# Performance work log

Measured on AMD Instinct MI355X. Metric: run time of the kernel, lower is better.

Reference implementation:

```python
import jax, jax.numpy as jnp
import numpy as np

N_CFG = 400_000    # total basic-block nodes across the batch
E_CFG = 1_600_000  # CFG edges
N_FUNC = 8_000     # internal functions across the batch
N_EXT = 1_600      # external functions across the batch
N_FCG = N_FUNC + N_EXT
E_FCG = 80_000     # call-graph edges
B = 8              # binaries per batch
D_IN, D_H = 64, 128
VOCAB = 10_002     # max_vocab_size + 2


def gcn_layer(x, edge_index, W, b, n_nodes):
    # PyG GCNConv with self-loops: x' = D^{-1/2}(A+I)D^{-1/2} (x W) + b
    h = x @ W
    row, col = edge_index[0], edge_index[1]
    deg = jax.ops.segment_sum(jnp.ones_like(col, dtype=h.dtype), col, num_segments=n_nodes) + 1.0
    dis = jax.lax.rsqrt(deg)
    norm = (dis[row] * dis[col])[:, None]
    agg = jax.ops.segment_sum(h[row] * norm, col, num_segments=n_nodes)
    return agg + h * (dis * dis)[:, None] + b  # second term is the self-loop message


def segment_mean(x, seg, n):
    s = jax.ops.segment_sum(x, seg, num_segments=n)
    c = jax.ops.segment_sum(jnp.ones((x.shape[0],), x.dtype), seg, num_segments=n)
    return s / jnp.maximum(c, 1.0)[:, None]


def setup_inputs() -> dict:
    key = jax.random.key(0)
    ks = jax.random.split(key, 24)
    s = 0.05
    cfg_x = jax.random.normal(ks[0], (N_CFG, D_IN), jnp.float32)
    cfg_edge_index = jax.random.randint(ks[1], (2, E_CFG), 0, N_CFG)
    cfg_node2func = jnp.sort(jax.random.randint(ks[2], (N_CFG,), 0, N_FUNC))
    fcg_edge_index = jax.random.randint(ks[3], (2, E_FCG), 0, N_FCG)
    fcg_batch = jnp.sort(jax.random.randint(ks[4], (N_FCG,), 0, B))
    # first N_FUNC FCG nodes are internal (index into pooled CFG embeddings),
    # the rest are external (index into the embedding table, avoiding pad idx 0)
    fcg_src_idx = jnp.concatenate([jnp.arange(N_FUNC, dtype=jnp.int64 if jax.config.jax_enable_x64 else jnp.int32).astype(jnp.int32),
                                   jax.random.randint(ks[5], (N_EXT,), 1, VOCAB)])
    fcg_is_ext = jnp.concatenate([jnp.zeros((N_FUNC,), jnp.int32), jnp.ones((N_EXT,), jnp.int32)])
    emb_table = jax.random.normal(ks[6], (VOCAB, D_H), jnp.float32) * s
    emb_table = emb_table.at[0].set(0.0)  # padding_idx row
    return {
        'cfg_x': cfg_x, 'cfg_edge_index': cfg_edge_index, 'cfg_node2func': cfg_node2func,
        'fcg_edge_index': fcg_edge_index, 'fcg_batch': fcg_batch,
        'fcg_src_idx': fcg_src_idx, 'fcg_is_ext': fcg_is_ext,
        'W_cfg1': jax.random.normal(ks[7], (D_IN, D_H), jnp.float32) * s,
        'b_cfg1': jax.random.normal(ks[8], (D_H,), jnp.float32) * s,
        'W_cfg2': jax.random.normal(ks[9], (D_H, D_H), jnp.float32) * s,
        'b_cfg2': jax.random.normal(ks[10], (D_H,), jnp.float32) * s,
        'emb_table': emb_table,
        'W_fcg1': jax.random.normal(ks[11], (D_H, D_H), jnp.float32) * s,
        'b_fcg1': jax.random.normal(ks[12], (D_H,), jnp.float32) * s,
        'Wp1': jax.random.normal(ks[13], (D_H, D_H // 2), jnp.float32) * s,
        'bp1': jax.random.normal(ks[14], (D_H // 2,), jnp.float32) * s,
        'Wp2': jax.random.normal(ks[15], (D_H // 2, D_H // 4), jnp.float32) * s,
        'bp2': jax.random.normal(ks[16], (D_H // 4,), jnp.float32) * s,
        'Wp3': jax.random.normal(ks[17], (D_H // 4, 1), jnp.float32) * s,
        'bp3': jax.random.normal(ks[18], (1,), jnp.float32) * s,
    }


def reference(cfg_x, cfg_edge_index, cfg_node2func, fcg_edge_index, fcg_batch,
              fcg_src_idx, fcg_is_ext, W_cfg1, b_cfg1, W_cfg2, b_cfg2, emb_table,
              W_fcg1, b_fcg1, Wp1, bp1, Wp2, bp2, Wp3, bp3):
    # CFG-level GCN stack (dropout is identity in eval)
    x = jax.nn.relu(gcn_layer(cfg_x, cfg_edge_index, W_cfg1, b_cfg1, N_CFG))
    x = jax.nn.relu(gcn_layer(x, cfg_edge_index, W_cfg2, b_cfg2, N_CFG))
    # global_mean_pool per function
    x_cfg_pool = segment_mean(x, cfg_node2func, N_FUNC)  # [N_FUNC, D_H]
    # assemble FCG node features: internal = pooled CFG embedding, external = embedding lookup
    internal = jnp.take(x_cfg_pool, jnp.clip(fcg_src_idx, 0, N_FUNC - 1), axis=0)
    external = jnp.take(emb_table, fcg_src_idx, axis=0, mode='clip')
    fcg_x = jnp.where((fcg_is_ext == 1)[:, None], external, internal)  # [N_FCG, D_H]
    # FCG-level GCN
    y = jax.nn.relu(gcn_layer(fcg_x, fcg_edge_index, W_fcg1, b_fcg1, N_FCG))
    # global_mean_pool per binary
    g = segment_mean(y, fcg_batch, B)  # [B, D_H]
    # projection head + sigmoid
    h = jax.nn.relu(g @ Wp1 + bp1)
    h = jax.nn.relu(h @ Wp2 + bp2)
    return jax.nn.sigmoid(h @ Wp3 + bp3)  # [B, 1]
```

## Files before the change

### kernel.cpp

```cpp
#include <hip/hip_runtime.h>
#include <math.h>

#define N_CFG 400000
#define E_CFG 1600000
#define N_FUNC 8000
#define N_EXT 1600
#define N_FCG (N_FUNC + N_EXT)
#define E_FCG 80000
#define NBATCH 8
#define VOCAB 10002

typedef unsigned int uint32;
typedef __attribute__((ext_vector_type(8))) short bf16x8;
typedef __attribute__((ext_vector_type(4))) float f32x4;

__device__ __forceinline__ float bf2f(unsigned short u){
  union { unsigned int i; float f; } v; v.i = ((unsigned int)u) << 16; return v.f;
}
__device__ __forceinline__ float bflo(unsigned int u){
  union { unsigned int i; float f; } v; v.i = u << 16; return v.f;
}
__device__ __forceinline__ float bfhi(unsigned int u){
  union { unsigned int i; float f; } v; v.i = u & 0xffff0000u; return v.f;
}
__device__ __forceinline__ unsigned short f2bf(float f){
  union { float f; unsigned int i; } v; v.f = f;
  unsigned int i = v.i;
  unsigned int r = (i + 0x7fffu + ((i >> 16) & 1u)) >> 16;
  return (unsigned short)r;
}
__device__ __forceinline__ unsigned int packbf(float x, float y){
  return (unsigned int)f2bf(x) | (((unsigned int)f2bf(y)) << 16);
}

__global__ void k_detect(const void* __restrict__ emb, int* __restrict__ flag){
  __shared__ int viol;
  if (threadIdx.x == 0) viol = 0;
  __syncthreads();
  const unsigned int* u = (const unsigned int*)emb;
  int my = 0;
  for (int i = threadIdx.x; i < 1024; i += 256){
    unsigned int lo = u[i] & 0xffffu;
    unsigned int ex = (lo >> 7) & 0xffu;
    bool ok = (ex == 0u) || (ex >= 80u && ex <= 127u);
    if (!ok) my++;
  }
  atomicAdd(&viol, my);
  __syncthreads();
  if (threadIdx.x == 0) *flag = (viol < 100) ? 1 : 0;
}

__global__ void k_conv(const void* __restrict__ src, unsigned short* __restrict__ dst,
                       int n, const int* __restrict__ flag){
  int i = blockIdx.x * 256 + threadIdx.x;
  if (i >= n) return;
  if (*flag) dst[i] = ((const unsigned short*)src)[i];
  else       dst[i] = f2bf(((const float*)src)[i]);
}

__global__ void k_convT(const void* __restrict__ src, unsigned short* __restrict__ dst,
                        int K, int N, const int* __restrict__ flag){
  int i = blockIdx.x * 256 + threadIdx.x;
  if (i >= K * N) return;
  int k = i / N, n = i - k * N;
  unsigned short v;
  if (*flag) v = ((const unsigned short*)src)[i];
  else       v = f2bf(((const float*)src)[i]);
  dst[n * K + k] = v;
}

__global__ void k_count(const int* __restrict__ idx, int n, uint32* __restrict__ cnt){
  int i = blockIdx.x * 256 + threadIdx.x;
  if (i < n) atomicAdd(&cnt[idx[i]], 1u);
}

__global__ void k_count_sorted(const int* __restrict__ seg, int n, uint32* __restrict__ cnt){
  int base = (blockIdx.x * 256 + threadIdx.x) * 64;
  if (base >= n) return;
  int end = base + 64; if (end > n) end = n;
  int curv = seg[base]; uint32 run = 1;
  for (int i = base + 1; i < end; i++){
    int v = seg[i];
    if (v == curv) run++;
    else { atomicAdd(&cnt[curv], run); curv = v; run = 1; }
  }
  atomicAdd(&cnt[curv], run);
}

__global__ void k_scan1(const uint32* __restrict__ cnt, int n,
                        uint32* __restrict__ off, uint32* __restrict__ bsums){
  __shared__ uint32 s[256];
  int tid = threadIdx.x;
  int base = blockIdx.x * 1024 + tid * 4;
  uint32 v0 = (base+0<n)?cnt[base+0]:0u, v1 = (base+1<n)?cnt[base+1]:0u;
  uint32 v2 = (base+2<n)?cnt[base+2]:0u, v3 = (base+3<n)?cnt[base+3]:0u;
  uint32 tsum = v0+v1+v2+v3;
  uint32 x = tsum;
  s[tid] = x; __syncthreads();
  for (int o = 1; o < 256; o <<= 1){
    uint32 y = (tid >= o) ? s[tid - o] : 0u;
    __syncthreads();
    x += y; s[tid] = x; __syncthreads();
  }
  uint32 run = x - tsum;
  if (base+0<n) off[base+0]=run; run+=v0;
  if (base+1<n) off[base+1]=run; run+=v1;
  if (base+2<n) off[base+2]=run; run+=v2;
  if (base+3<n) off[base+3]=run;
  if (tid == 255) bsums[blockIdx.x] = x;
}

__global__ void k_scan2(uint32* bsums, int nb){
  __shared__ uint32 s[1024];
  int tid = threadIdx.x;
  uint32 v = (tid < nb) ? bsums[tid] : 0u;
  uint32 x = v;
  s[tid] = x; __syncthreads();
  for (int o = 1; o < 1024; o <<= 1){
    uint32 y = (tid >= o) ? s[tid - o] : 0u;
    __syncthreads();
    x += y; s[tid] = x; __syncthreads();
  }
  if (tid < nb) bsums[tid] = x - v;
}

__global__ void k_scan3(uint32* off, uint32* cur, const uint32* __restrict__ bsums, int n){
  int i = blockIdx.x * 256 + threadIdx.x;
  if (i >= n) return;
  uint32 v = off[i] + bsums[i >> 10];
  off[i] = v;
  if (cur) cur[i] = v;
}

__global__ void k_fill(const int* __restrict__ edges, int E,
                       uint32* __restrict__ cur, int* __restrict__ sorted){
  int e = blockIdx.x * 256 + threadIdx.x;
  if (e >= E) return;
  int r = edges[e];
  int c = edges[E + e];
  uint32 p = atomicAdd(&cur[c], 1u);
  sorted[p] = r;
}

__global__ void k_dis(const uint32* __restrict__ cnt, float* __restrict__ dis, int n){
  int i = blockIdx.x * 256 + threadIdx.x;
  if (i < n) dis[i] = rsqrtf((float)cnt[i] + 1.0f);
}

template<int K>
__global__ __launch_bounds__(256)
void k_gemm_mfma(const void* __restrict__ Xsrc, const unsigned short* __restrict__ Wt,
                 const float* __restrict__ dis, unsigned short* __restrict__ out,
                 const int* __restrict__ flag, int mixed){
  const int KP = K + 8;
  __shared__ unsigned short Xs[64 * (K + 8)];
  __shared__ unsigned short Ws[128 * (K + 8)];
  int tid = threadIdx.x;
  long row0 = (long)blockIdx.x * 64;

  {
    int n = tid >> 1, half = tid & 1;
    const uint4* src = (const uint4*)(Wt + n * K) + half * (K / 16);
    uint4* dst = (uint4*)(Ws + n * KP) + half * (K / 16);
    #pragma unroll
    for (int i = 0; i < K / 16; i++) dst[i] = src[i];
  }
  {
    int r = tid >> 2, part = tid & 3;
    int isbf = mixed ? *flag : 1;
    uint4* dst = (uint4*)(Xs + r * KP) + part * (K / 32);
    if (isbf){
      const uint4* src = (const uint4*)((const unsigned short*)Xsrc + (row0 + r) * K) + part * (K / 32);
      #pragma unroll
      for (int i = 0; i < K / 32; i++) dst[i] = src[i];
    } else {
      const float4* src = (const float4*)((const float*)Xsrc + (row0 + r) * K) + part * (K / 16);
      #pragma unroll
      for (int i = 0; i < K / 32; i++){
        float4 f0 = src[2*i], f1 = src[2*i+1];
        uint4 u;
        u.x = packbf(f0.x, f0.y); u.y = packbf(f0.z, f0.w);
        u.z = packbf(f1.x, f1.y); u.w = packbf(f1.z, f1.w);
        dst[i] = u;
      }
    }
  }
  __syncthreads();

  int w = tid >> 6, lane = tid & 63, m = lane & 15, q = lane >> 4;
  f32x4 acc[8];
  #pragma unroll
  for (int t = 0; t < 8; t++) acc[t] = (f32x4){0.f, 0.f, 0.f, 0.f};

  const unsigned short* Arow = &Xs[(w * 16 + m) * KP + q * 8];
  const unsigned short* Bbase = &Ws[m * KP + q * 8];
  #pragma unroll
  for (int kc = 0; kc < K; kc += 32){
    bf16x8 a = *(const bf16x8*)(Arow + kc);
    #pragma unroll
    for (int t = 0; t < 8; t++){
      bf16x8 b = *(const bf16x8*)(Bbase + t * 16 * KP + kc);
      acc[t] = __builtin_amdgcn_mfma_f32_16x16x32_bf16(a, b, acc[t], 0, 0, 0);
    }
  }

  float d[4];
  #pragma unroll
  for (int r = 0; r < 4; r++) d[r] = dis[row0 + w * 16 + q * 4 + r];
  #pragma unroll
  for (int t = 0; t < 8; t++){
    #pragma unroll
    for (int r = 0; r < 4; r++){
      long grow = row0 + w * 16 + q * 4 + r;
      out[grow * 128 + t * 16 + m] = f2bf(acc[t][r] * d[r]);
    }
  }
}

__global__ __launch_bounds__(256)
void k_agg4(const uint4* __restrict__ hs4,
            const uint32* __restrict__ off, const uint32* __restrict__ cnt,
            const int* __restrict__ sorted, const float* __restrict__ dis,
            const uint4* __restrict__ bias4, uint4* __restrict__ out4, int n){
  int tid = threadIdx.x;
  int wave = tid >> 6, lane = tid & 63, grp = lane >> 4, sub = lane & 15;
  int node = blockIdx.x * 16 + wave * 4 + grp;
  if (node >= n) return;
  uint32 o = off[node], c = cnt[node];
  float a[8] = {0.f,0.f,0.f,0.f,0.f,0.f,0.f,0.f};
  for (uint32 j = 0; j < c; j++){
    int r = sorted[o + j];
    uint4 u = hs4[(long)r * 16 + sub];
    a[0] += bflo(u.x); a[1] += bfhi(u.x);
    a[2] += bflo(u.y); a[3] += bfhi(u.y);
    a[4] += bflo(u.z); a[5] += bfhi(u.z);
    a[6] += bflo(u.w); a[7] += bfhi(u.w);
  }
  {
    uint4 u = hs4[(long)node * 16 + sub];
    a[0] += bflo(u.x); a[1] += bfhi(u.x);
    a[2] += bflo(u.y); a[3] += bfhi(u.y);
    a[4] += bflo(u.z); a[5] += bfhi(u.z);
    a[6] += bflo(u.w); a[7] += bfhi(u.w);
  }
  float d = dis[node];
  uint4 b = bias4[sub];
  float v0 = fmaxf(fmaf(d, a[0], bflo(b.x)), 0.f);
  float v1 = fmaxf(fmaf(d, a[1], bfhi(b.x)), 0.f);
  float v2 = fmaxf(fmaf(d, a[2], bflo(b.y)), 0.f);
  float v3 = fmaxf(fmaf(d, a[3], bfhi(b.y)), 0.f);
  float v4 = fmaxf(fmaf(d, a[4], bflo(b.z)), 0.f);
  float v5 = fmaxf(fmaf(d, a[5], bfhi(b.z)), 0.f);
  float v6 = fmaxf(fmaf(d, a[6], bflo(b.w)), 0.f);
  float v7 = fmaxf(fmaf(d, a[7], bfhi(b.w)), 0.f);
  uint4 ov;
  ov.x = packbf(v0, v1); ov.y = packbf(v2, v3);
  ov.z = packbf(v4, v5); ov.w = packbf(v6, v7);
  out4[(long)node * 16 + sub] = ov;
}

__global__ __launch_bounds__(256)
void k_pool_batch(const uint4* __restrict__ y4, const uint32* __restrict__ g_cnt,
                  float* __restrict__ g_sum){
  __shared__ float red[16][128];
  int b = blockIdx.x >> 3, s = blockIdx.x & 7;
  int tid = threadIdx.x;
  int grp = tid >> 4, sub = tid & 15;
  uint32 start = 0;
  for (int i = 0; i < b; i++) start += g_cnt[i];
  uint32 cb = g_cnt[b];
  uint32 len = (cb + 7) / 8;
  uint32 lo = s * len;
  uint32 hi = lo + len; if (hi > cb) hi = cb;
  float a[8] = {0.f,0.f,0.f,0.f,0.f,0.f,0.f,0.f};
  for (uint32 i = lo + grp; i < hi; i += 16){
    uint4 u = y4[(long)(start + i) * 16 + sub];
    a[0] += bflo(u.x); a[1] += bfhi(u.x);
    a[2] += bflo(u.y); a[3] += bfhi(u.y);
    a[4] += bflo(u.z); a[5] += bfhi(u.z);
    a[6] += bflo(u.w); a[7] += bfhi(u.w);
  }
  #pragma unroll
  for (int i = 0; i < 8; i++) red[grp][sub * 8 + i] = a[i];
  __syncthreads();
  if (tid < 128){
    float t = 0.f;
    #pragma unroll
    for (int g = 0; g < 16; g++) t += red[g][tid];
    atomicAdd(&g_sum[b * 128 + tid], t);
  }
}

__global__ void k_pool_mean(const unsigned int* __restrict__ x2, const uint32* __restrict__ off,
                            const uint32* __restrict__ cnt, unsigned int* __restrict__ pooled2, int nf){
  int f = blockIdx.x; int t = threadIdx.x;
  uint32 o = off[f], c = cnt[f];
  float sx = 0.f, sy = 0.f;
  for (uint32 j = 0; j < c; j++){
    unsigned int u = x2[(long)(o + j) * 64 + t];
    sx += bflo(u); sy += bfhi(u);
  }
  float inv = 1.0f / (float)((c > 0u) ? c : 1u);
  pooled2[(long)f * 64 + t] = packbf(sx * inv, sy * inv);
}

__global__ void k_assemble(const unsigned int* __restrict__ pooled2, const unsigned int* __restrict__ emb2,
                           const int* __restrict__ src, const int* __restrict__ isext,
                           unsigned int* __restrict__ fx2){
  int i = blockIdx.x; int t = threadIdx.x;
  int s = src[i];
  unsigned int v;
  if (isext[i] == 1){
    int idx = s; if (idx < 0) idx = 0; if (idx > VOCAB - 1) idx = VOCAB - 1;
    v = emb2[(long)idx * 64 + t];
  } else {
    int f = s; if (f < 0) f = 0; if (f > N_FUNC - 1) f = N_FUNC - 1;
    v = pooled2[(long)f * 64 + t];
  }
  fx2[(long)i * 64 + t] = v;
}

__global__ __launch_bounds__(256)
void k_head(const float* __restrict__ g_sum, const uint32* __restrict__ g_cnt,
            const unsigned short* __restrict__ Wp1, const unsigned short* __restrict__ bp1,
            const unsigned short* __restrict__ Wp2, const unsigned short* __restrict__ bp2,
            const unsigned short* __restrict__ Wp3, const unsigned short* __restrict__ bp3,
            void* __restrict__ outp, const int* __restrict__ flag){
  __shared__ float G[8 * 128];
  __shared__ float H1[8 * 64];
  __shared__ float H2[8 * 32];
  int tid = threadIdx.x;
  for (int i = tid; i < 1024; i += 256){
    uint32 c = g_cnt[i >> 7];
    G[i] = g_sum[i] / (float)((c > 0u) ? c : 1u);
  }
  __syncthreads();
  for (int i = tid; i < 512; i += 256){
    int b = i >> 6, j = i & 63;
    float a = bf2f(bp1[j]);
    for (int d = 0; d < 128; d++) a = fmaf(G[b * 128 + d], bf2f(Wp1[d * 64 + j]), a);
    H1[i] = fmaxf(a, 0.f);
  }
  __syncthreads();
  {
    int b = tid >> 5, j = tid & 31;
    float a = bf2f(bp2[j]);
    for (int d = 0; d < 64; d++) a = fmaf(H1[b * 64 + d], bf2f(Wp2[d * 32 + j]), a);
    H2[tid] = fmaxf(a, 0.f);
  }
  __syncthreads();
  if (tid < 8){
    float a = bf2f(bp3[0]);
    for (int d = 0; d < 32; d++) a = fmaf(H2[tid * 32 + d], bf2f(Wp3[d]), a);
    float s = 1.f / (1.f + __expf(-a));
    if (*flag) ((unsigned short*)outp)[tid] = f2bf(s);
    else       ((float*)outp)[tid] = s;
  }
}

extern "C" void kernel_launch(void* const* d_in, const int* in_sizes, int n_in,
                              void* d_out, int out_size, void* d_ws, size_t ws_size,
                              hipStream_t stream){
  const void* cfg_x     = d_in[0];
  const int*  cfg_edges = (const int*)d_in[1];
  const int*  node2func = (const int*)d_in[2];
  const int*  fcg_edges = (const int*)d_in[3];
  const int*  fcg_batch = (const int*)d_in[4];
  const int*  fcg_src   = (const int*)d_in[5];
  const int*  fcg_isext = (const int*)d_in[6];
  const void* W1  = d_in[7];
  const void* b1  = d_in[8];
  const void* W2  = d_in[9];
  const void* b2  = d_in[10];
  const void* emb = d_in[11];
  const void* Wf  = d_in[12];
  const void* bfv = d_in[13];
  const void* Wp1 = d_in[14];
  const void* bp1 = d_in[15];
  const void* Wp2 = d_in[16];
  const void* bp2 = d_in[17];
  const void* Wp3 = d_in[18];
  const void* bp3 = d_in[19];

  char* p = (char*)d_ws;
  auto carve = [&](size_t bytes)->char* {
    char* r = p; p += (bytes + 255) & ~(size_t)255; return r;
  };
  unsigned short* A   = (unsigned short*)carve((size_t)N_CFG * 128 * 2);
  unsigned short* Bx  = (unsigned short*)carve((size_t)N_CFG * 128 * 2);
  uint32* cnt_cfg = (uint32*)carve((size_t)N_CFG * 4);
  uint32* off_cfg = (uint32*)carve((size_t)N_CFG * 4);
  uint32* cur_cfg = (uint32*)carve((size_t)N_CFG * 4);
  float*  dis_cfg = (float*) carve((size_t)N_CFG * 4);
  int*    sorted_cfg = (int*)carve((size_t)E_CFG * 4);
  uint32* bsums   = (uint32*)carve(1024 * 4);
  uint32* pool_cnt = (uint32*)carve(N_FUNC * 4);
  uint32* pool_off = (uint32*)carve(N_FUNC * 4);
  unsigned int* pooled2 = (unsigned int*)carve((size_t)N_FUNC * 64 * 4);
  unsigned int* fx2     = (unsigned int*)carve((size_t)N_FCG * 64 * 4);
  unsigned short* hsf   = (unsigned short*)carve((size_t)N_FCG * 128 * 2);
  unsigned short* yf    = (unsigned short*)carve((size_t)N_FCG * 128 * 2);
  uint32* cnt_f = (uint32*)carve(N_FCG * 4);
  uint32* off_f = (uint32*)carve(N_FCG * 4);
  uint32* cur_f = (uint32*)carve(N_FCG * 4);
  float*  dis_f = (float*) carve(N_FCG * 4);
  int*    sorted_f = (int*)carve(E_FCG * 4);
  float*  g_sum = (float*)carve(8 * 128 * 4);
  uint32* g_cnt = (uint32*)carve(8 * 4);
  int*    flag  = (int*)   carve(256);
  unsigned short* cW1t = (unsigned short*)carve(128 * 64 * 2);
  unsigned short* cb1  = (unsigned short*)carve(128 * 2);
  unsigned short* cW2t = (unsigned short*)carve(128 * 128 * 2);
  unsigned short* cb2  = (unsigned short*)carve(128 * 2);
  unsigned short* cemb = (unsigned short*)carve((size_t)VOCAB * 128 * 2);
  unsigned short* cWft = (unsigned short*)carve(128 * 128 * 2);
  unsigned short* cbf  = (unsigned short*)carve(128 * 2);
  unsigned short* cWp1 = (unsigned short*)carve(128 * 64 * 2);
  unsigned short* cbp1 = (unsigned short*)carve(64 * 2);
  unsigned short* cWp2 = (unsigned short*)carve(64 * 32 * 2);
  unsigned short* cbp2 = (unsigned short*)carve(32 * 2);
  unsigned short* cWp3 = (unsigned short*)carve(32 * 2);
  unsigned short* cbp3 = (unsigned short*)carve(2 * 2);

  hipMemsetAsync(cnt_cfg, 0, (size_t)N_CFG * 4, stream);
  hipMemsetAsync(cnt_f,   0, (size_t)N_FCG * 4, stream);
  hipMemsetAsync(pool_cnt,0, (size_t)N_FUNC * 4, stream);
  hipMemsetAsync(g_sum,   0, 8 * 128 * 4, stream);
  hipMemsetAsync(g_cnt,   0, 8 * 4, stream);

  k_detect<<<1, 256, 0, stream>>>(emb, flag);
  auto conv = [&](const void* src, unsigned short* dst, int n){
    k_conv<<<(n + 255) / 256, 256, 0, stream>>>(src, dst, n, flag);
  };
  k_convT<<<(64 * 128 + 255) / 256, 256, 0, stream>>>(W1, cW1t, 64, 128, flag);
  k_convT<<<(128 * 128 + 255) / 256, 256, 0, stream>>>(W2, cW2t, 128, 128, flag);
  k_convT<<<(128 * 128 + 255) / 256, 256, 0, stream>>>(Wf, cWft, 128, 128, flag);
  conv(b1, cb1, 128);
  conv(b2, cb2, 128);
  conv(emb, cemb, VOCAB * 128);
  conv(bfv, cbf, 128);
  conv(Wp1, cWp1, 128 * 64); conv(bp1, cbp1, 64);
  conv(Wp2, cWp2, 64 * 32);  conv(bp2, cbp2, 32);
  conv(Wp3, cWp3, 32);       conv(bp3, cbp3, 1);

  k_count<<<(E_CFG + 255) / 256, 256, 0, stream>>>(cfg_edges + E_CFG, E_CFG, cnt_cfg);
  int nb_cfg = (N_CFG + 1023) / 1024;
  k_scan1<<<nb_cfg, 256, 0, stream>>>(cnt_cfg, N_CFG, off_cfg, bsums);
  k_scan2<<<1, 1024, 0, stream>>>(bsums, nb_cfg);
  k_scan3<<<(N_CFG + 255) / 256, 256, 0, stream>>>(off_cfg, cur_cfg, bsums, N_CFG);
  k_fill<<<(E_CFG + 255) / 256, 256, 0, stream>>>(cfg_edges, E_CFG, cur_cfg, sorted_cfg);
  k_dis<<<(N_CFG + 255) / 256, 256, 0, stream>>>(cnt_cfg, dis_cfg, N_CFG);

  k_gemm_mfma<64><<<N_CFG / 64, 256, 0, stream>>>(cfg_x, cW1t, dis_cfg, A, flag, 1);
  k_agg4<<<N_CFG / 16, 256, 0, stream>>>((const uint4*)A, off_cfg, cnt_cfg, sorted_cfg,
                                         dis_cfg, (const uint4*)cb1, (uint4*)Bx, N_CFG);
  k_gemm_mfma<128><<<N_CFG / 64, 256, 0, stream>>>(Bx, cW2t, dis_cfg, A, flag, 0);
  k_agg4<<<N_CFG / 16, 256, 0, stream>>>((const uint4*)A, off_cfg, cnt_cfg, sorted_cfg,
                                         dis_cfg, (const uint4*)cb2, (uint4*)Bx, N_CFG);

  k_count_sorted<<<((N_CFG + 63) / 64 + 255) / 256, 256, 0, stream>>>(node2func, N_CFG, pool_cnt);
  int nb_pool = (N_FUNC + 1023) / 1024;
  k_scan1<<<nb_pool, 256, 0, stream>>>(pool_cnt, N_FUNC, pool_off, bsums);
  k_scan2<<<1, 1024, 0, stream>>>(bsums, nb_pool);
  k_scan3<<<(N_FUNC + 255) / 256, 256, 0, stream>>>(pool_off, (uint32*)nullptr, bsums, N_FUNC);
  k_pool_mean<<<N_FUNC, 64, 0, stream>>>((const unsigned int*)Bx, pool_off, pool_cnt, pooled2, N_FUNC);

  k_assemble<<<N_FCG, 64, 0, stream>>>(pooled2, (const unsigned int*)cemb, fcg_src, fcg_isext, fx2);

  k_count<<<(E_FCG + 255) / 256, 256, 0, stream>>>(fcg_edges + E_FCG, E_FCG, cnt_f);
  int nb_f = (N_FCG + 1023) / 1024;
  k_scan1<<<nb_f, 256, 0, stream>>>(cnt_f, N_FCG, off_f, bsums);
  k_scan2<<<1, 1024, 0, stream>>>(bsums, nb_f);
  k_scan3<<<(N_FCG + 255) / 256, 256, 0, stream>>>(off_f, cur_f, bsums, N_FCG);
  k_fill<<<(E_FCG + 255) / 256, 256, 0, stream>>>(fcg_edges, E_FCG, cur_f, sorted_f);
  k_dis<<<(N_FCG + 255) / 256, 256, 0, stream>>>(cnt_f, dis_f, N_FCG);

  k_gemm_mfma<128><<<N_FCG / 64, 256, 0, stream>>>((const void*)fx2, cWft, dis_f, hsf, flag, 0);
  k_count_sorted<<<1, 256, 0, stream>>>(fcg_batch, N_FCG, g_cnt);
  k_agg4<<<N_FCG / 16, 256, 0, stream>>>((const uint4*)hsf, off_f, cnt_f, sorted_f,
                                         dis_f, (const uint4*)cbf, (uint4*)yf, N_FCG);
  k_pool_batch<<<64, 256, 0, stream>>>((const uint4*)yf, g_cnt, g_sum);

  k_head<<<1, 256, 0, stream>>>(g_sum, g_cnt, cWp1, cbp1, cWp2, cbp2, cWp3, cbp3, d_out, flag);
}
```

Baseline: 786.3 us.

## Reorder GCN to aggregate-then-transform, fuse setup and scans, single-pass CSR builds

Reorders each GCN layer so neighbour aggregation runs on the input features first and the GEMM follows, with bias and ReLU fused into the GEMM epilogue. The first layer therefore gathers 64-wide rows instead of 128-wide ones. The many conversion and memset launches are merged into one grid-stride init kernel. The three-pass scan is replaced by a decoupled-lookback single-pass scan that also writes the cursor and degree arrays. The CFG edge fill is split into two column windows, the FCG CSR is built in one shared-memory block, pooling offsets come from binary search, and batch pooling is fused with the head. This cuts launch count and gather traffic, but the lookback spin and the single-block CSR kernel add serialisation risk.

```diff
diff --git a/kernel.cpp b/kernel.cpp
--- a/kernel.cpp
+++ b/kernel.cpp
@@ -11,6 +11,7 @@
 #define VOCAB 10002
 
 typedef unsigned int uint32;
+typedef unsigned long long ull;
 typedef __attribute__((ext_vector_type(8))) short bf16x8;
 typedef __attribute__((ext_vector_type(4))) float f32x4;
 
@@ -32,41 +33,74 @@
 __device__ __forceinline__ unsigned int packbf(float x, float y){
   return (unsigned int)f2bf(x) | (((unsigned int)f2bf(y)) << 16);
 }
-
-__global__ void k_detect(const void* __restrict__ emb, int* __restrict__ flag){
+__device__ __forceinline__ int lowerb(const int* __restrict__ a, int n, int key){
+  int lo = 0, hi = n;
+  while (lo < hi){ int mid = (lo + hi) >> 1; if (a[mid] < key) lo = mid + 1; else hi = mid; }
+  return lo;
+}
+
+struct InitParams {
+  const void *cfg_x, *W1, *W2, *Wf, *b1, *b2, *bfv, *emb, *Wp1, *bp1, *Wp2, *bp2, *Wp3, *bp3;
+  unsigned short *cx, *cW1t, *cW2t, *cWft, *cb1, *cb2, *cbf, *cemb, *cWp1, *cbp1, *cWp2, *cbp2, *cWp3, *cbp3;
+  uint32 *cnt_cfg; ull* state; uint32* ticket; uint32* done; int* flag;
+};
+
+#define CVLOOP(srcp, dstp, nn) \
+  for (long i = gid; i < (nn); i += gsz) \
+    (dstp)[i] = isbf ? ((const unsigned short*)(srcp))[i] : f2bf(((const float*)(srcp))[i]);
+
+__global__ __launch_bounds__(256)
+void k_init(InitParams P){
   __shared__ int viol;
-  if (threadIdx.x == 0) viol = 0;
-  __syncthreads();
-  const unsigned int* u = (const unsigned int*)emb;
+  int tid = threadIdx.x;
+  if (tid == 0) viol = 0;
+  __syncthreads();
+  const unsigned int* eu = (const unsigned int*)P.emb;
   int my = 0;
-  for (int i = threadIdx.x; i < 1024; i += 256){
-    unsigned int lo = u[i] & 0xffffu;
+  for (int i = tid; i < 1024; i += 256){
+    unsigned int lo = eu[i] & 0xffffu;
     unsigned int ex = (lo >> 7) & 0xffu;
-    bool ok = (ex == 0u) || (ex >= 80u && ex <= 127u);
-    if (!ok) my++;
+    if (!((ex == 0u) || (ex >= 80u && ex <= 127u))) my++;
   }
   atomicAdd(&viol, my);
   __syncthreads();
-  if (threadIdx.x == 0) *flag = (viol < 100) ? 1 : 0;
-}
-
-__global__ void k_conv(const void* __restrict__ src, unsigned short* __restrict__ dst,
-                       int n, const int* __restrict__ flag){
-  int i = blockIdx.x * 256 + threadIdx.x;
-  if (i >= n) return;
-  if (*flag) dst[i] = ((const unsigned short*)src)[i];
-  else       dst[i] = f2bf(((const float*)src)[i]);
-}
-
-__global__ void k_convT(const void* __restrict__ src, unsigned short* __restrict__ dst,
-                        int K, int N, const int* __restrict__ flag){
-  int i = blockIdx.x * 256 + threadIdx.x;
-  if (i >= K * N) return;
-  int k = i / N, n = i - k * N;
-  unsigned short v;
-  if (*flag) v = ((const unsigned short*)src)[i];
-  else       v = f2bf(((const float*)src)[i]);
-  dst[n * K + k] = v;
+  int isbf = (viol < 100) ? 1 : 0;
+  long gid = (long)blockIdx.x * 256 + tid;
+  long gsz = (long)gridDim.x * 256;
+  if (gid == 0){ *P.flag = isbf; *P.ticket = 0u; *P.done = 0u; }
+  for (long i = gid; i < 400; i += gsz) P.state[i] = 0ULL;
+  uint4 z4 = {0u,0u,0u,0u};
+  for (long i = gid; i < N_CFG/4; i += gsz) ((uint4*)P.cnt_cfg)[i] = z4;
+  long nx8 = (long)N_CFG * 64 / 8;
+  for (long i = gid; i < nx8; i += gsz){
+    uint4 o;
+    if (isbf){
+      o = ((const uint4*)P.cfg_x)[i];
+    } else {
+      const float4* f = (const float4*)P.cfg_x + i * 2;
+      float4 f0 = f[0], f1 = f[1];
+      o.x = packbf(f0.x, f0.y); o.y = packbf(f0.z, f0.w);
+      o.z = packbf(f1.x, f1.y); o.w = packbf(f1.z, f1.w);
+    }
+    ((uint4*)P.cx)[i] = o;
+  }
+  CVLOOP(P.emb, P.cemb, (long)VOCAB * 128);
+  for (long i = gid; i < 64 * 128; i += gsz){
+    int k = i >> 7, n = i & 127;
+    unsigned short v = isbf ? ((const unsigned short*)P.W1)[i] : f2bf(((const float*)P.W1)[i]);
+    P.cW1t[n * 64 + k] = v;
+  }
+  for (long i = gid; i < 128 * 128; i += gsz){
+    int k = i >> 7, n = i & 127;
+    unsigned short v = isbf ? ((const unsigned short*)P.W2)[i] : f2bf(((const float*)P.W2)[i]);
+    P.cW2t[n * 128 + k] = v;
+    unsigned short w = isbf ? ((const unsigned short*)P.Wf)[i] : f2bf(((const float*)P.Wf)[i]);
+    P.cWft[n * 128 + k] = w;
+  }
+  CVLOOP(P.b1, P.cb1, 128); CVLOOP(P.b2, P.cb2, 128); CVLOOP(P.bfv, P.cbf, 128);
+  CVLOOP(P.Wp1, P.cWp1, 8192); CVLOOP(P.bp1, P.cbp1, 64);
+  CVLOOP(P.Wp2, P.cWp2, 2048); CVLOOP(P.bp2, P.cbp2, 32);
+  CVLOOP(P.Wp3, P.cWp3, 32);   CVLOOP(P.bp3, P.cbp3, 1);
 }
 
 __global__ void k_count(const int* __restrict__ idx, int n, uint32* __restrict__ cnt){
@@ -74,90 +108,120 @@
   if (i < n) atomicAdd(&cnt[idx[i]], 1u);
 }
 
-__global__ void k_count_sorted(const int* __restrict__ seg, int n, uint32* __restrict__ cnt){
-  int base = (blockIdx.x * 256 + threadIdx.x) * 64;
-  if (base >= n) return;
-  int end = base + 64; if (end > n) end = n;
-  int curv = seg[base]; uint32 run = 1;
-  for (int i = base + 1; i < end; i++){
-    int v = seg[i];
-    if (v == curv) run++;
-    else { atomicAdd(&cnt[curv], run); curv = v; run = 1; }
-  }
-  atomicAdd(&cnt[curv], run);
-}
-
-__global__ void k_scan1(const uint32* __restrict__ cnt, int n,
-                        uint32* __restrict__ off, uint32* __restrict__ bsums){
+__global__ __launch_bounds__(256)
+void k_scan_lb(const uint32* __restrict__ cnt, int n,
+               uint32* __restrict__ off, uint32* __restrict__ cur, float* __restrict__ dis,
+               ull* __restrict__ state, uint32* __restrict__ ticket){
   __shared__ uint32 s[256];
+  __shared__ uint32 tshare, bshare;
   int tid = threadIdx.x;
-  int base = blockIdx.x * 1024 + tid * 4;
+  if (tid == 0) tshare = atomicAdd(ticket, 1u);
+  __syncthreads();
+  uint32 t = tshare;
+  int base = (int)t * 1024 + tid * 4;
   uint32 v0 = (base+0<n)?cnt[base+0]:0u, v1 = (base+1<n)?cnt[base+1]:0u;
   uint32 v2 = (base+2<n)?cnt[base+2]:0u, v3 = (base+3<n)?cnt[base+3]:0u;
-  uint32 tsum = v0+v1+v2+v3;
-  uint32 x = tsum;
+  uint32 tsum = v0+v1+v2+v3, x = tsum;
   s[tid] = x; __syncthreads();
   for (int o = 1; o < 256; o <<= 1){
     uint32 y = (tid >= o) ? s[tid - o] : 0u;
     __syncthreads();
     x += y; s[tid] = x; __syncthreads();
   }
-  uint32 run = x - tsum;
-  if (base+0<n) off[base+0]=run; run+=v0;
-  if (base+1<n) off[base+1]=run; run+=v1;
-  if (base+2<n) off[base+2]=run; run+=v2;
-  if (base+3<n) off[base+3]=run;
-  if (tid == 255) bsums[blockIdx.x] = x;
-}
-
-__global__ void k_scan2(uint32* bsums, int nb){
-  __shared__ uint32 s[1024];
-  int tid = threadIdx.x;
-  uint32 v = (tid < nb) ? bsums[tid] : 0u;
-  uint32 x = v;
-  s[tid] = x; __syncthreads();
-  for (int o = 1; o < 1024; o <<= 1){
-    uint32 y = (tid >= o) ? s[tid - o] : 0u;
-    __syncthreads();
-    x += y; s[tid] = x; __syncthreads();
-  }
-  if (tid < nb) bsums[tid] = x - v;
-}
-
-__global__ void k_scan3(uint32* off, uint32* cur, const uint32* __restrict__ bsums, int n){
-  int i = blockIdx.x * 256 + threadIdx.x;
-  if (i >= n) return;
-  uint32 v = off[i] + bsums[i >> 10];
-  off[i] = v;
-  if (cur) cur[i] = v;
-}
-
-__global__ void k_fill(const int* __restrict__ edges, int E,
-                       uint32* __restrict__ cur, int* __restrict__ sorted){
+  uint32 total = s[255];
+  if (tid == 0){
+    if (t == 0){
+      atomicExch(&state[0], (2ULL << 32) | (ull)total);
+      bshare = 0u;
+    } else {
+      atomicExch(&state[t], (1ULL << 32) | (ull)total);
+      uint32 run = 0; int idx = (int)t - 1;
+      while (true){
+        ull sv = atomicAdd(&state[idx], 0ULL);
+        uint32 st = (uint32)(sv >> 32);
+        if (st == 0u){ __builtin_amdgcn_s_sleep(1); continue; }
+        run += (uint32)sv;
+        if (st == 2u) break;
+        idx--;
+      }
+      atomicExch(&state[t], (2ULL << 32) | (ull)(run + total));
+      bshare = run;
+    }
+  }
+  __syncthreads();
+  uint32 run = bshare + (x - tsum);
+  if (base+0<n){ off[base+0]=run; cur[base+0]=run; dis[base+0]=rsqrtf((float)v0+1.f); } run+=v0;
+  if (base+1<n){ off[base+1]=run; cur[base+1]=run; dis[base+1]=rsqrtf((float)v1+1.f); } run+=v1;
+  if (base+2<n){ off[base+2]=run; cur[base+2]=run; dis[base+2]=rsqrtf((float)v2+1.f); } run+=v2;
+  if (base+3<n){ off[base+3]=run; cur[base+3]=run; dis[base+3]=rsqrtf((float)v3+1.f); }
+}
+
+__global__ void k_fill_win(const int* __restrict__ edges, int E,
+                           uint32* __restrict__ cur, int* __restrict__ sorted,
+                           int lo, int hi){
   int e = blockIdx.x * 256 + threadIdx.x;
   if (e >= E) return;
+  int c = edges[E + e];
+  if (c < lo || c >= hi) return;
   int r = edges[e];
-  int c = edges[E + e];
   uint32 p = atomicAdd(&cur[c], 1u);
   sorted[p] = r;
 }
 
-__global__ void k_dis(const uint32* __restrict__ cnt, float* __restrict__ dis, int n){
-  int i = blockIdx.x * 256 + threadIdx.x;
-  if (i < n) dis[i] = rsqrtf((float)cnt[i] + 1.0f);
+#define ACCD(u, d) { \
+  a[0] = fmaf(d, bflo(u.x), a[0]); a[1] = fmaf(d, bfhi(u.x), a[1]); \
+  a[2] = fmaf(d, bflo(u.y), a[2]); a[3] = fmaf(d, bfhi(u.y), a[3]); \
+  a[4] = fmaf(d, bflo(u.z), a[4]); a[5] = fmaf(d, bfhi(u.z), a[5]); \
+  a[6] = fmaf(d, bflo(u.w), a[6]); a[7] = fmaf(d, bfhi(u.w), a[7]); }
+
+template<int LPN>
+__global__ __launch_bounds__(256)
+void k_aggZ(const uint4* __restrict__ x4, const uint32* __restrict__ off,
+            const uint32* __restrict__ cnt, const int* __restrict__ sorted,
+            const float* __restrict__ dis, uint4* __restrict__ z4, int n){
+  int tid = threadIdx.x;
+  int grp = tid / LPN, sub = tid % LPN;
+  int node = blockIdx.x * (256 / LPN) + grp;
+  if (node >= n) return;
+  uint32 o = off[node], c = cnt[node];
+  float a[8] = {0.f,0.f,0.f,0.f,0.f,0.f,0.f,0.f};
+  uint32 j = 0;
+  for (; j + 3 < c; j += 4){
+    int r0 = sorted[o+j], r1 = sorted[o+j+1], r2 = sorted[o+j+2], r3 = sorted[o+j+3];
+    float d0 = dis[r0], d1 = dis[r1], d2 = dis[r2], d3 = dis[r3];
+    uint4 u0 = x4[(long)r0 * LPN + sub];
+    uint4 u1 = x4[(long)r1 * LPN + sub];
+    uint4 u2 = x4[(long)r2 * LPN + sub];
+    uint4 u3 = x4[(long)r3 * LPN + sub];
+    ACCD(u0, d0); ACCD(u1, d1); ACCD(u2, d2); ACCD(u3, d3);
+  }
+  for (; j < c; j++){
+    int r = sorted[o + j];
+    float d = dis[r];
+    uint4 u = x4[(long)r * LPN + sub];
+    ACCD(u, d);
+  }
+  {
+    float d = dis[node];
+    uint4 u = x4[(long)node * LPN + sub];
+    ACCD(u, d);
+  }
+  uint4 ov;
+  ov.x = packbf(a[0], a[1]); ov.y = packbf(a[2], a[3]);
+  ov.z = packbf(a[4], a[5]); ov.w = packbf(a[6], a[7]);
+  z4[(long)node * LPN + sub] = ov;
 }
 
 template<int K>
 __global__ __launch_bounds__(256)
-void k_gemm_mfma(const void* __restrict__ Xsrc, const unsigned short* __restrict__ Wt,
-                 const float* __restrict__ dis, unsigned short* __restrict__ out,
-                 const int* __restrict__ flag, int mixed){
+void k_gemm_relu(const unsigned short* __restrict__ X, const unsigned short* __restrict__ Wt,
+                 const float* __restrict__ dis, const unsigned short* __restrict__ bias,
+                 unsigned short* __restrict__ out){
   const int KP = K + 8;
   __shared__ unsigned short Xs[64 * (K + 8)];
   __shared__ unsigned short Ws[128 * (K + 8)];
   int tid = threadIdx.x;
   long row0 = (long)blockIdx.x * 64;
-
   {
     int n = tid >> 1, half = tid & 1;
     const uint4* src = (const uint4*)(Wt + n * K) + half * (K / 16);
@@ -167,23 +231,10 @@
   }
   {
     int r = tid >> 2, part = tid & 3;
-    int isbf = mixed ? *flag : 1;
+    const uint4* src = (const uint4*)(X + (row0 + r) * K) + part * (K / 32);
     uint4* dst = (uint4*)(Xs + r * KP) + part * (K / 32);
-    if (isbf){
-      const uint4* src = (const uint4*)((const unsigned short*)Xsrc + (row0 + r) * K) + part * (K / 32);
-      #pragma unroll
-      for (int i = 0; i < K / 32; i++) dst[i] = src[i];
-    } else {
-      const float4* src = (const float4*)((const float*)Xsrc + (row0 + r) * K) + part * (K / 16);
-      #pragma unroll
-      for (int i = 0; i < K / 32; i++){
-        float4 f0 = src[2*i], f1 = src[2*i+1];
-        uint4 u;
-        u.x = packbf(f0.x, f0.y); u.y = packbf(f0.z, f0.w);
-        u.z = packbf(f1.x, f1.y); u.w = packbf(f1.z, f1.w);
-        dst[i] = u;
-      }
-    }
+    #pragma unroll
+    for (int i = 0; i < K / 32; i++) dst[i] = src[i];
   }
   __syncthreads();
 
@@ -191,7 +242,6 @@
   f32x4 acc[8];
   #pragma unroll
   for (int t = 0; t < 8; t++) acc[t] = (f32x4){0.f, 0.f, 0.f, 0.f};
-
   const unsigned short* Arow = &Xs[(w * 16 + m) * KP + q * 8];
   const unsigned short* Bbase = &Ws[m * KP + q * 8];
   #pragma unroll
@@ -203,104 +253,32 @@
       acc[t] = __builtin_amdgcn_mfma_f32_16x16x32_bf16(a, b, acc[t], 0, 0, 0);
     }
   }
-
   float d[4];
   #pragma unroll
   for (int r = 0; r < 4; r++) d[r] = dis[row0 + w * 16 + q * 4 + r];
   #pragma unroll
   for (int t = 0; t < 8; t++){
+    float bc = bf2f(bias[t * 16 + m]);
     #pragma unroll
     for (int r = 0; r < 4; r++){
       long grow = row0 + w * 16 + q * 4 + r;
-      out[grow * 128 + t * 16 + m] = f2bf(acc[t][r] * d[r]);
+      out[grow * 128 + t * 16 + m] = f2bf(fmaxf(fmaf(d[r], acc[t][r], bc), 0.f));
     }
   }
 }
 
-__global__ __launch_bounds__(256)
-void k_agg4(const uint4* __restrict__ hs4,
-            const uint32* __restrict__ off, const uint32* __restrict__ cnt,
-            const int* __restrict__ sorted, const float* __restrict__ dis,
-            const uint4* __restrict__ bias4, uint4* __restrict__ out4, int n){
-  int tid = threadIdx.x;
-  int wave = tid >> 6, lane = tid & 63, grp = lane >> 4, sub = lane & 15;
-  int node = blockIdx.x * 16 + wave * 4 + grp;
-  if (node >= n) return;
-  uint32 o = off[node], c = cnt[node];
-  float a[8] = {0.f,0.f,0.f,0.f,0.f,0.f,0.f,0.f};
-  for (uint32 j = 0; j < c; j++){
-    int r = sorted[o + j];
-    uint4 u = hs4[(long)r * 16 + sub];
-    a[0] += bflo(u.x); a[1] += bfhi(u.x);
-    a[2] += bflo(u.y); a[3] += bfhi(u.y);
-    a[4] += bflo(u.z); a[5] += bfhi(u.z);
-    a[6] += bflo(u.w); a[7] += bfhi(u.w);
-  }
-  {
-    uint4 u = hs4[(long)node * 16 + sub];
-    a[0] += bflo(u.x); a[1] += bfhi(u.x);
-    a[2] += bflo(u.y); a[3] += bfhi(u.y);
-    a[4] += bflo(u.z); a[5] += bfhi(u.z);
-    a[6] += bflo(u.w); a[7] += bfhi(u.w);
-  }
-  float d = dis[node];
-  uint4 b = bias4[sub];
-  float v0 = fmaxf(fmaf(d, a[0], bflo(b.x)), 0.f);
-  float v1 = fmaxf(fmaf(d, a[1], bfhi(b.x)), 0.f);
-  float v2 = fmaxf(fmaf(d, a[2], bflo(b.y)), 0.f);
-  float v3 = fmaxf(fmaf(d, a[3], bfhi(b.y)), 0.f);
-  float v4 = fmaxf(fmaf(d, a[4], bflo(b.z)), 0.f);
-  float v5 = fmaxf(fmaf(d, a[5], bfhi(b.z)), 0.f);
-  float v6 = fmaxf(fmaf(d, a[6], bflo(b.w)), 0.f);
-  float v7 = fmaxf(fmaf(d, a[7], bfhi(b.w)), 0.f);
-  uint4 ov;
-  ov.x = packbf(v0, v1); ov.y = packbf(v2, v3);
-  ov.z = packbf(v4, v5); ov.w = packbf(v6, v7);
-  out4[(long)node * 16 + sub] = ov;
-}
-
-__global__ __launch_bounds__(256)
-void k_pool_batch(const uint4* __restrict__ y4, const uint32* __restrict__ g_cnt,
-                  float* __restrict__ g_sum){
-  __shared__ float red[16][128];
-  int b = blockIdx.x >> 3, s = blockIdx.x & 7;
-  int tid = threadIdx.x;
-  int grp = tid >> 4, sub = tid & 15;
-  uint32 start = 0;
-  for (int i = 0; i < b; i++) start += g_cnt[i];
-  uint32 cb = g_cnt[b];
-  uint32 len = (cb + 7) / 8;
-  uint32 lo = s * len;
-  uint32 hi = lo + len; if (hi > cb) hi = cb;
-  float a[8] = {0.f,0.f,0.f,0.f,0.f,0.f,0.f,0.f};
-  for (uint32 i = lo + grp; i < hi; i += 16){
-    uint4 u = y4[(long)(start + i) * 16 + sub];
-    a[0] += bflo(u.x); a[1] += bfhi(u.x);
-    a[2] += bflo(u.y); a[3] += bfhi(u.y);
-    a[4] += bflo(u.z); a[5] += bfhi(u.z);
-    a[6] += bflo(u.w); a[7] += bfhi(u.w);
-  }
-  #pragma unroll
-  for (int i = 0; i < 8; i++) red[grp][sub * 8 + i] = a[i];
-  __syncthreads();
-  if (tid < 128){
-    float t = 0.f;
-    #pragma unroll
-    for (int g = 0; g < 16; g++) t += red[g][tid];
-    atomicAdd(&g_sum[b * 128 + tid], t);
-  }
-}
-
-__global__ void k_pool_mean(const unsigned int* __restrict__ x2, const uint32* __restrict__ off,
-                            const uint32* __restrict__ cnt, unsigned int* __restrict__ pooled2, int nf){
+__global__ void k_pool_mean(const unsigned int* __restrict__ x2, const int* __restrict__ n2f,
+                            unsigned int* __restrict__ pooled2){
   int f = blockIdx.x; int t = threadIdx.x;
-  uint32 o = off[f], c = cnt[f];
+  int s = lowerb(n2f, N_CFG, f);
+  int e = lowerb(n2f, N_CFG, f + 1);
   float sx = 0.f, sy = 0.f;
-  for (uint32 j = 0; j < c; j++){
-    unsigned int u = x2[(long)(o + j) * 64 + t];
+  for (int j = s; j < e; j++){
+    unsigned int u = x2[(long)j * 64 + t];
     sx += bflo(u); sy += bfhi(u);
   }
-  float inv = 1.0f / (float)((c > 0u) ? c : 1u);
+  int c = e - s;
+  float inv = 1.0f / (float)((c > 0) ? c : 1);
   pooled2[(long)f * 64 + t] = packbf(sx * inv, sy * inv);
 }
 
@@ -320,41 +298,123 @@
   fx2[(long)i * 64 + t] = v;
 }
 
+__global__ __launch_bounds__(1024)
+void k_fcg_csr(const int* __restrict__ edges, uint32* __restrict__ cnt_f,
+               uint32* __restrict__ off_f, float* __restrict__ dis_f,
+               int* __restrict__ sorted_f){
+  __shared__ uint32 scnt[N_FCG];
+  __shared__ uint32 stmp[1024];
+  int tid = threadIdx.x;
+  for (int i = tid; i < N_FCG; i += 1024) scnt[i] = 0u;
+  __syncthreads();
+  for (int e = tid; e < E_FCG; e += 1024) atomicAdd(&scnt[edges[E_FCG + e]], 1u);
+  __syncthreads();
+  uint32 local[10], s = 0;
+  #pragma unroll
+  for (int k = 0; k < 10; k++){
+    int idx = tid * 10 + k;
+    uint32 v = (idx < N_FCG) ? scnt[idx] : 0u;
+    local[k] = s; s += v;
+  }
+  uint32 x = s;
+  stmp[tid] = x; __syncthreads();
+  for (int o = 1; o < 1024; o <<= 1){
+    uint32 y = (tid >= o) ? stmp[tid - o] : 0u;
+    __syncthreads();
+    x += y; stmp[tid] = x; __syncthreads();
+  }
+  uint32 excl = x - s;
+  uint32 offv[10];
+  #pragma unroll
+  for (int k = 0; k < 10; k++){
+    int idx = tid * 10 + k;
+    if (idx < N_FCG){
+      uint32 cv = scnt[idx];
+      uint32 ov = excl + local[k];
+      offv[k] = ov;
+      cnt_f[idx] = cv;
+      off_f[idx] = ov;
+      dis_f[idx] = rsqrtf((float)cv + 1.0f);
+    }
+  }
+  __syncthreads();
+  #pragma unroll
+  for (int k = 0; k < 10; k++){
+    int idx = tid * 10 + k;
+    if (idx < N_FCG) scnt[idx] = offv[k];
+  }
+  __syncthreads();
+  for (int e = tid; e < E_FCG; e += 1024){
+    int c = edges[E_FCG + e];
+    int r = edges[e];
+    uint32 p = atomicAdd(&scnt[c], 1u);
+    sorted_f[p] = r;
+  }
+}
+
 __global__ __launch_bounds__(256)
-void k_head(const float* __restrict__ g_sum, const uint32* __restrict__ g_cnt,
-            const unsigned short* __restrict__ Wp1, const unsigned short* __restrict__ bp1,
-            const unsigned short* __restrict__ Wp2, const unsigned short* __restrict__ bp2,
-            const unsigned short* __restrict__ Wp3, const unsigned short* __restrict__ bp3,
-            void* __restrict__ outp, const int* __restrict__ flag){
-  __shared__ float G[8 * 128];
-  __shared__ float H1[8 * 64];
-  __shared__ float H2[8 * 32];
-  int tid = threadIdx.x;
-  for (int i = tid; i < 1024; i += 256){
-    uint32 c = g_cnt[i >> 7];
-    G[i] = g_sum[i] / (float)((c > 0u) ? c : 1u);
-  }
+void k_pool_head(const uint4* __restrict__ y4, const int* __restrict__ batch,
+                 float* __restrict__ G, uint32* __restrict__ done,
+                 const unsigned short* __restrict__ Wp1, const unsigned short* __restrict__ bp1,
+                 const unsigned short* __restrict__ Wp2, const unsigned short* __restrict__ bp2,
+                 const unsigned short* __restrict__ Wp3, const unsigned short* __restrict__ bp3,
+                 void* __restrict__ outp, const int* __restrict__ flag){
+  __shared__ float red[16][128];
+  __shared__ uint32 tick;
+  int b = blockIdx.x, tid = threadIdx.x;
+  int s = lowerb(batch, N_FCG, b);
+  int e = lowerb(batch, N_FCG, b + 1);
+  int grp = tid >> 4, sub = tid & 15;
+  float a[8] = {0.f,0.f,0.f,0.f,0.f,0.f,0.f,0.f};
+  for (int i = s + grp; i < e; i += 16){
+    uint4 u = y4[(long)i * 16 + sub];
+    a[0] += bflo(u.x); a[1] += bfhi(u.x);
+    a[2] += bflo(u.y); a[3] += bfhi(u.y);
+    a[4] += bflo(u.z); a[5] += bfhi(u.z);
+    a[6] += bflo(u.w); a[7] += bfhi(u.w);
+  }
+  #pragma unroll
+  for (int i = 0; i < 8; i++) red[grp][sub * 8 + i] = a[i];
+  __syncthreads();
+  int c = e - s;
+  float inv = 1.0f / (float)((c > 0) ? c : 1);
+  if (tid < 128){
+    float t2 = 0.f;
+    #pragma unroll
+    for (int g = 0; g < 16; g++) t2 += red[g][tid];
+    atomicExch((unsigned int*)&G[b * 128 + tid], __float_as_uint(t2 * inv));
+  }
+  __threadfence();
+  __syncthreads();
+  if (tid == 0) tick = atomicAdd(done, 1u);
+  __syncthreads();
+  if (tick != NBATCH - 1) return;
+  __shared__ float Gs[1024];
+  __shared__ float H1[512];
+  __shared__ float H2[256];
+  for (int i = tid; i < 1024; i += 256)
+    Gs[i] = __uint_as_float(atomicAdd((unsigned int*)&G[i], 0u));
   __syncthreads();
   for (int i = tid; i < 512; i += 256){
-    int b = i >> 6, j = i & 63;
-    float a = bf2f(bp1[j]);
-    for (int d = 0; d < 128; d++) a = fmaf(G[b * 128 + d], bf2f(Wp1[d * 64 + j]), a);
-    H1[i] = fmaxf(a, 0.f);
+    int bb = i >> 6, j = i & 63;
+    float acc = bf2f(bp1[j]);
+    for (int d = 0; d < 128; d++) acc = fmaf(Gs[bb * 128 + d], bf2f(Wp1[d * 64 + j]), acc);
+    H1[i] = fmaxf(acc, 0.f);
   }
   __syncthreads();
   {
-    int b = tid >> 5, j = tid & 31;
-    float a = bf2f(bp2[j]);
-    for (int d = 0; d < 64; d++) a = fmaf(H1[b * 64 + d], bf2f(Wp2[d * 32 + j]), a);
-    H2[tid] = fmaxf(a, 0.f);
+    int bb = tid >> 5, j = tid & 31;
+    float acc = bf2f(bp2[j]);
+    for (int d = 0; d < 64; d++) acc = fmaf(H1[bb * 64 + d], bf2f(Wp2[d * 32 + j]), acc);
+    H2[tid] = fmaxf(acc, 0.f);
   }
   __syncthreads();
   if (tid < 8){
-    float a = bf2f(bp3[0]);
-    for (int d = 0; d < 32; d++) a = fmaf(H2[tid * 32 + d], bf2f(Wp3[d]), a);
-    float s = 1.f / (1.f + __expf(-a));
-    if (*flag) ((unsigned short*)outp)[tid] = f2bf(s);
-    else       ((float*)outp)[tid] = s;
+    float acc = bf2f(bp3[0]);
+    for (int d = 0; d < 32; d++) acc = fmaf(H2[tid * 32 + d], bf2f(Wp3[d]), acc);
+    float sg = 1.f / (1.f + __expf(-acc));
+    if (*flag) ((unsigned short*)outp)[tid] = f2bf(sg);
+    else       ((float*)outp)[tid] = sg;
   }
 }
 
@@ -368,19 +428,6 @@
   const int*  fcg_batch = (const int*)d_in[4];
   const int*  fcg_src   = (const int*)d_in[5];
   const int*  fcg_isext = (const int*)d_in[6];
-  const void* W1  = d_in[7];
-  const void* b1  = d_in[8];
-  const void* W2  = d_in[9];
-  const void* b2  = d_in[10];
-  const void* emb = d_in[11];
-  const void* Wf  = d_in[12];
-  const void* bfv = d_in[13];
-  const void* Wp1 = d_in[14];
-  const void* bp1 = d_in[15];
-  const void* Wp2 = d_in[16];
-  const void* bp2 = d_in[17];
-  const void* Wp3 = d_in[18];
-  const void* bp3 = d_in[19];
 
   char* p = (char*)d_ws;
   auto carve = [&](size_t bytes)->char* {
@@ -388,26 +435,25 @@
   };
   unsigned short* A   = (unsigned short*)carve((size_t)N_CFG * 128 * 2);
   unsigned short* Bx  = (unsigned short*)carve((size_t)N_CFG * 128 * 2);
+  unsigned short* cx  = (unsigned short*)carve((size_t)N_CFG * 64 * 2);
   uint32* cnt_cfg = (uint32*)carve((size_t)N_CFG * 4);
   uint32* off_cfg = (uint32*)carve((size_t)N_CFG * 4);
   uint32* cur_cfg = (uint32*)carve((size_t)N_CFG * 4);
   float*  dis_cfg = (float*) carve((size_t)N_CFG * 4);
   int*    sorted_cfg = (int*)carve((size_t)E_CFG * 4);
-  uint32* bsums   = (uint32*)carve(1024 * 4);
-  uint32* pool_cnt = (uint32*)carve(N_FUNC * 4);
-  uint32* pool_off = (uint32*)carve(N_FUNC * 4);
+  ull*    state = (ull*)carve(400 * 8);
+  uint32* ticket = (uint32*)carve(256);
+  uint32* done   = (uint32*)carve(256);
+  int*    flag   = (int*)carve(256);
   unsigned int* pooled2 = (unsigned int*)carve((size_t)N_FUNC * 64 * 4);
   unsigned int* fx2     = (unsigned int*)carve((size_t)N_FCG * 64 * 4);
-  unsigned short* hsf   = (unsigned short*)carve((size_t)N_FCG * 128 * 2);
+  unsigned short* Zf    = (unsigned short*)carve((size_t)N_FCG * 128 * 2);
   unsigned short* yf    = (unsigned short*)carve((size_t)N_FCG * 128 * 2);
   uint32* cnt_f = (uint32*)carve(N_FCG * 4);
   uint32* off_f = (uint32*)carve(N_FCG * 4);
-  uint32* cur_f = (uint32*)carve(N_FCG * 4);
   float*  dis_f = (float*) carve(N_FCG * 4);
   int*    sorted_f = (int*)carve(E_FCG * 4);
-  float*  g_sum = (float*)carve(8 * 128 * 4);
-  uint32* g_cnt = (uint32*)carve(8 * 4);
-  int*    flag  = (int*)   carve(256);
+  float*  G = (float*)carve(8 * 128 * 4);
   unsigned short* cW1t = (unsigned short*)carve(128 * 64 * 2);
   unsigned short* cb1  = (unsigned short*)carve(128 * 2);
   unsigned short* cW2t = (unsigned short*)carve(128 * 128 * 2);
@@ -422,64 +468,40 @@
   unsigned short* cWp3 = (unsigned short*)carve(32 * 2);
   unsigned short* cbp3 = (unsigned short*)carve(2 * 2);
 
-  hipMemsetAsync(cnt_cfg, 0, (size_t)N_CFG * 4, stream);
-  hipMemsetAsync(cnt_f,   0, (size_t)N_FCG * 4, stream);
-  hipMemsetAsync(pool_cnt,0, (size_t)N_FUNC * 4, stream);
-  hipMemsetAsync(g_sum,   0, 8 * 128 * 4, stream);
-  hipMemsetAsync(g_cnt,   0, 8 * 4, stream);
-
-  k_detect<<<1, 256, 0, stream>>>(emb, flag);
-  auto conv = [&](const void* src, unsigned short* dst, int n){
-    k_conv<<<(n + 255) / 256, 256, 0, stream>>>(src, dst, n, flag);
-  };
-  k_convT<<<(64 * 128 + 255) / 256, 256, 0, stream>>>(W1, cW1t, 64, 128, flag);
-  k_convT<<<(128 * 128 + 255) / 256, 256, 0, stream>>>(W2, cW2t, 128, 128, flag);
-  k_convT<<<(128 * 128 + 255) / 256, 256, 0, stream>>>(Wf, cWft, 128, 128, flag);
-  conv(b1, cb1, 128);
-  conv(b2, cb2, 128);
-  conv(emb, cemb, VOCAB * 128);
-  conv(bfv, cbf, 128);
-  conv(Wp1, cWp1, 128 * 64); conv(bp1, cbp1, 64);
-  conv(Wp2, cWp2, 64 * 32);  conv(bp2, cbp2, 32);
-  conv(Wp3, cWp3, 32);       conv(bp3, cbp3, 1);
+  InitParams P;
+  P.cfg_x = cfg_x; P.W1 = d_in[7]; P.W2 = d_in[9]; P.Wf = d_in[12];
+  P.b1 = d_in[8]; P.b2 = d_in[10]; P.bfv = d_in[13]; P.emb = d_in[11];
+  P.Wp1 = d_in[14]; P.bp1 = d_in[15]; P.Wp2 = d_in[16]; P.bp2 = d_in[17];
+  P.Wp3 = d_in[18]; P.bp3 = d_in[19];
+  P.cx = cx; P.cW1t = cW1t; P.cW2t = cW2t; P.cWft = cWft;
+  P.cb1 = cb1; P.cb2 = cb2; P.cbf = cbf; P.cemb = cemb;
+  P.cWp1 = cWp1; P.cbp1 = cbp1; P.cWp2 = cWp2; P.cbp2 = cbp2;
+  P.cWp3 = cWp3; P.cbp3 = cbp3;
+  P.cnt_cfg = cnt_cfg; P.state = state; P.ticket = ticket; P.done = done; P.flag = flag;
+  k_init<<<2048, 256, 0, stream>>>(P);
 
   k_count<<<(E_CFG + 255) / 256, 256, 0, stream>>>(cfg_edges + E_CFG, E_CFG, cnt_cfg);
-  int nb_cfg = (N_CFG + 1023) / 1024;
-  k_scan1<<<nb_cfg, 256, 0, stream>>>(cnt_cfg, N_CFG, off_cfg, bsums);
-  k_scan2<<<1, 1024, 0, stream>>>(bsums, nb_cfg);
-  k_scan3<<<(N_CFG + 255) / 256, 256, 0, stream>>>(off_cfg, cur_cfg, bsums, N_CFG);
-  k_fill<<<(E_CFG + 255) / 256, 256, 0, stream>>>(cfg_edges, E_CFG, cur_cfg, sorted_cfg);
-  k_dis<<<(N_CFG + 255) / 256, 256, 0, stream>>>(cnt_cfg, dis_cfg, N_CFG);
-
-  k_gemm_mfma<64><<<N_CFG / 64, 256, 0, stream>>>(cfg_x, cW1t, dis_cfg, A, flag, 1);
-  k_agg4<<<N_CFG / 16, 256, 0, stream>>>((const uint4*)A, off_cfg, cnt_cfg, sorted_cfg,
-                                         dis_cfg, (const uint4*)cb1, (uint4*)Bx, N_CFG);
-  k_gemm_mfma<128><<<N_CFG / 64, 256, 0, stream>>>(Bx, cW2t, dis_cfg, A, flag, 0);
-  k_agg4<<<N_CFG / 16, 256, 0, stream>>>((const uint4*)A, off_cfg, cnt_cfg, sorted_cfg,
-                                         dis_cfg, (const uint4*)cb2, (uint4*)Bx, N_CFG);
-
-  k_count_sorted<<<((N_CFG + 63) / 64 + 255) / 256, 256, 0, stream>>>(node2func, N_CFG, pool_cnt);
-  int nb_pool = (N_FUNC + 1023) / 1024;
-  k_scan1<<<nb_pool, 256, 0, stream>>>(pool_cnt, N_FUNC, pool_off, bsums);
-  k_scan2<<<1, 1024, 0, stream>>>(bsums, nb_pool);
-  k_scan3<<<(N_FUNC + 255) / 256, 256, 0, stream>>>(pool_off, (uint32*)nullptr, bsums, N_FUNC);
-  k_pool_mean<<<N_FUNC, 64, 0, stream>>>((const unsigned int*)Bx, pool_off, pool_cnt, pooled2, N_FUNC);
-
+  k_scan_lb<<<(N_CFG + 1023) / 1024, 256, 0, stream>>>(cnt_cfg, N_CFG, off_cfg, cur_cfg, dis_cfg,
+                                                       state, ticket);
+  for (int w = 0; w < 2; w++)
+    k_fill_win<<<(E_CFG + 255) / 256, 256, 0, stream>>>(cfg_edges, E_CFG, cur_cfg, sorted_cfg,
+                                                        w * (N_CFG / 2), (w + 1) * (N_CFG / 2));
+
+  k_aggZ<8><<<N_CFG / 32, 256, 0, stream>>>((const uint4*)cx, off_cfg, cnt_cfg, sorted_cfg,
+                                            dis_cfg, (uint4*)A, N_CFG);
+  k_gemm_relu<64><<<N_CFG / 64, 256, 0, stream>>>(A, cW1t, dis_cfg, cb1, Bx);
+
+  k_aggZ<16><<<N_CFG / 16, 256, 0, stream>>>((const uint4*)Bx, off_cfg, cnt_cfg, sorted_cfg,
+                                             dis_cfg, (uint4*)A, N_CFG);
+  k_gemm_relu<128><<<N_CFG / 64, 256, 0, stream>>>(A, cW2t, dis_cfg, cb2, Bx);
+
+  k_pool_mean<<<N_FUNC, 64, 0, stream>>>((const unsigned int*)Bx, node2func, pooled2);
   k_assemble<<<N_FCG, 64, 0, stream>>>(pooled2, (const unsigned int*)cemb, fcg_src, fcg_isext, fx2);
 
-  k_count<<<(E_FCG + 255) / 256, 256, 0, stream>>>(fcg_edges + E_FCG, E_FCG, cnt_f);
-  int nb_f = (N_FCG + 1023) / 1024;
-  k_scan1<<<nb_f, 256, 0, stream>>>(cnt_f, N_FCG, off_f, bsums);
-  k_scan2<<<1, 1024, 0, stream>>>(bsums, nb_f);
-  k_scan3<<<(N_FCG + 255) / 256, 256, 0, stream>>>(off_f, cur_f, bsums, N_FCG);
-  k_fill<<<(E_FCG + 255) / 256, 256, 0, stream>>>(fcg_edges, E_FCG, cur_f, sorted_f);
-  k_dis<<<(N_FCG + 255) / 256, 256, 0, stream>>>(cnt_f, dis_f, N_FCG);
-
-  k_gemm_mfma<128><<<N_FCG / 64, 256, 0, stream>>>((const void*)fx2, cWft, dis_f, hsf, flag, 0);
-  k_count_sorted<<<1, 256, 0, stream>>>(fcg_batch, N_FCG, g_cnt);
-  k_agg4<<<N_FCG / 16, 256, 0, stream>>>((const uint4*)hsf, off_f, cnt_f, sorted_f,
-                                         dis_f, (const uint4*)cbf, (uint4*)yf, N_FCG);
-  k_pool_batch<<<64, 256, 0, stream>>>((const uint4*)yf, g_cnt, g_sum);
-
-  k_head<<<1, 256, 0, stream>>>(g_sum, g_cnt, cWp1, cbp1, cWp2, cbp2, cWp3, cbp3, d_out, flag);
-}
+  k_fcg_csr<<<1, 1024, 0, stream>>>(fcg_edges, cnt_f, off_f, dis_f, sorted_f);
+  k_aggZ<16><<<N_FCG / 16, 256, 0, stream>>>((const uint4*)fx2, off_f, cnt_f, sorted_f,
+                                             dis_f, (uint4*)Zf, N_FCG);
+  k_gemm_relu<128><<<N_FCG / 64, 256, 0, stream>>>(Zf, cWft, dis_f, cbf, yf);
+  k_pool_head<<<NBATCH, 256, 0, stream>>>((const uint4*)yf, fcg_batch, G, done,
+                                          cWp1, cbp1, cWp2, cbp2, cWp3, cbp3, d_out, flag);
+}
```

Result: slower. 878.7 us (+11.8%).
